# Optimization experiments

Measured on AMD Instinct MI355X. Metric: run time of the kernel, lower is better.

## Reference

```python
import jax, jax.numpy as jnp
import numpy as np

B, S, D, H = 2, 2048, 1024, 16
HD = D // H


def setup_inputs() -> dict:
    key = jax.random.key(0)
    ks = jax.random.split(key, 12)
    s = 0.02
    inp = {
        "query": jax.random.normal(ks[0], (B, S, D), dtype=jnp.float32),
        "Wq": jax.random.normal(ks[1], (D, D), dtype=jnp.float32) * s,
        "bq": jnp.zeros((D,), jnp.float32),
        "Wk": jax.random.normal(ks[2], (D, D), dtype=jnp.float32) * s,
        "bk": jnp.zeros((D,), jnp.float32),
        "Wv": jax.random.normal(ks[3], (D, D), dtype=jnp.float32) * s,
        "bv": jnp.zeros((D,), jnp.float32),
        "Wo": jax.random.normal(ks[4], (D, D), dtype=jnp.float32) * s,
        "bo": jnp.zeros((D,), jnp.float32),
        "Wm1": jax.random.normal(ks[5], (D // 4, D), dtype=jnp.float32) * s,
        "bm1": jnp.zeros((D // 4,), jnp.float32),
        "Wm2": jax.random.normal(ks[6], (D, D // 4), dtype=jnp.float32) * s,
        "bm2": jnp.zeros((D,), jnp.float32),
        "dopamine": jnp.ones((1,), jnp.float32),
        "serotonin": jnp.ones((1,), jnp.float32),
        "norepinephrine": jnp.ones((1,), jnp.float32),
        "acetylcholine": jnp.ones((1,), jnp.float32),
        "attention_scale": jnp.ones((1,), jnp.float32),
        "attention_bias": jnp.zeros((1,), jnp.float32),
    }
    return inp


def reference(query, Wq, bq, Wk, bk, Wv, bv, Wo, bo, Wm1, bm1, Wm2, bm2,
              dopamine, serotonin, norepinephrine, acetylcholine,
              attention_scale, attention_bias):
    b, s, d = query.shape
    scale = HD ** -0.5
    split = lambda t: t.reshape(b, s, H, HD).transpose(0, 2, 1, 3)  # [b,h,s,hd]
    q = split(query @ Wq.T + bq)
    k = split(query @ Wk.T + bk)
    v = split(query @ Wv.T + bv)
    scores = jnp.einsum('bhqd,bhkd->bhqk', q, k) * scale
    w = jax.nn.softmax(scores, axis=-1)  # dropout=0 (eval)
    attn = jnp.einsum('bhqk,bhkd->bhqd', w, v)
    # neuromodulation MLP on flattened query, then combined scalar gate
    mod = jax.nn.relu(query @ Wm1.T + bm1) @ Wm2.T + bm2  # [b,s,d]
    gate = (dopamine + serotonin + norepinephrine + acetylcholine) / 4.0  # [1]
    neuro = split(mod * gate)  # [b,h,s,hd]
    attn = (attn * attention_scale + attention_bias) * (1.0 + neuro)
    out = attn.transpose(0, 2, 1, 3).reshape(b, s, d) @ Wo.T + bo
    return out
```

## Files before the change

kernel.cpp:

```cpp
#include <hip/hip_runtime.h>
#include <hip/hip_bf16.h>
#include <stdint.h>
#include <math.h>


typedef __attribute__((ext_vector_type(8))) short short8;
typedef __attribute__((ext_vector_type(8))) unsigned short ushort8;
typedef __attribute__((ext_vector_type(4))) float floatx4;

#define MFMA16(a, b, c) __builtin_amdgcn_mfma_f32_16x16x32_bf16(a, b, c, 0, 0, 0)

__device__ __forceinline__ unsigned short f2bf(float f) {
    union { float f; uint32_t u; } v; v.f = f;
    uint32_t r = v.u + 0x7fffu + ((v.u >> 16) & 1u);
    return (unsigned short)(r >> 16);
}
__device__ __forceinline__ float bf2f(unsigned short s) {
    union { uint32_t u; float f; } v; v.u = ((uint32_t)s) << 16;
    return v.f;
}
__device__ __forceinline__ uint32_t pk2(float a, float b) {
    __hip_bfloat162 t = __float22bfloat162_rn(make_float2(a, b));
    uint32_t u; __builtin_memcpy(&u, &t, 4); return u;
}

typedef const __attribute__((address_space(1))) void gvoid_t;
typedef __attribute__((address_space(3))) void lvoid_t;
__device__ __forceinline__ void gld16(const void* g, void* l) {
    __builtin_amdgcn_global_load_lds((gvoid_t*)g, (lvoid_t*)l, 16, 0, 0);
}

template<bool OUTBF>
__device__ __forceinline__ void gemm_core128(const unsigned short* __restrict__ A,
                                             const unsigned short* __restrict__ W,
                                             const float* __restrict__ bias,
                                             void* __restrict__ C,
                                             int N, int K, int bm, int bn,
                                             bool relu, float osc,
                                             unsigned short* __restrict__ vt)
{
    __shared__ __align__(16) unsigned short As[2][128][32];
    __shared__ __align__(16) unsigned short Ws[2][128][32];

    const int tid  = threadIdx.x;
    const int w    = tid >> 6, lane = tid & 63;
    const int ln   = lane & 15, quad = lane >> 4;
    const int wm   = (w >> 1) * 64, wn = (w & 1) * 64;

    floatx4 acc[4][4] = {};

    auto stage = [&](int k0, int bb) {
        #pragma unroll
        for (int i = 0; i < 4; i++) {
            const int t = w * 4 + i;
            if (t < 8) {
                const int r0  = t * 16;
                const int row = r0 + (lane >> 2);
                const int c   = (lane & 3) ^ ((row >> 1) & 3);
                gld16(&A[(size_t)(bm + row) * K + k0 + c * 8], &As[bb][r0][0]);
            } else {
                const int r0  = (t - 8) * 16;
                const int row = r0 + (lane >> 2);
                const int c   = (lane & 3) ^ ((row >> 1) & 3);
                gld16(&W[(size_t)(bn + row) * K + k0 + c * 8], &Ws[bb][r0][0]);
            }
        }
    };

    stage(0, 0);

    const int KI = K >> 5;
    for (int ki = 0; ki < KI; ki++) {
        const int bb = ki & 1;
        __syncthreads();
        if (ki + 1 < KI) stage((ki + 1) << 5, bb ^ 1);

        short8 af[4], bf[4];
        #pragma unroll
        for (int mt = 0; mt < 4; mt++) {
            const int row = wm + mt * 16 + ln;
            af[mt] = *(const short8*)&As[bb][row][(quad ^ ((row >> 1) & 3)) * 8];
        }
        #pragma unroll
        for (int nt = 0; nt < 4; nt++) {
            const int row = wn + nt * 16 + ln;
            bf[nt] = *(const short8*)&Ws[bb][row][(quad ^ ((row >> 1) & 3)) * 8];
        }
        #pragma unroll
        for (int mt = 0; mt < 4; mt++)
            #pragma unroll
            for (int nt = 0; nt < 4; nt++)
                acc[mt][nt] = MFMA16(af[mt], bf[nt], acc[mt][nt]);
    }

    float bv[4];
    #pragma unroll
    for (int nt = 0; nt < 4; nt++) bv[nt] = bias[bn + wn + nt * 16 + ln];

    if (vt != nullptr) {
        #pragma unroll
        for (int mt = 0; mt < 4; mt++) {
            const int rowg = bm + wm + mt * 16 + quad * 4;
            const int b = rowg >> 11, s = rowg & 2047;
            #pragma unroll
            for (int nt = 0; nt < 4; nt++) {
                const int n = bn + wn + nt * 16 + ln;
                const int h = n >> 6, hd = n & 63;
                uint2 pk;
                pk.x = pk2(acc[mt][nt][0] + bv[nt], acc[mt][nt][1] + bv[nt]);
                pk.y = pk2(acc[mt][nt][2] + bv[nt], acc[mt][nt][3] + bv[nt]);
                *(uint2*)&vt[((size_t)(b * 16 + h) * 64 + hd) * 2048 + s] = pk;
            }
        }
        return;
    }

    #pragma unroll
    for (int mt = 0; mt < 4; mt++) {
        #pragma unroll
        for (int nt = 0; nt < 4; nt++) {
            #pragma unroll
            for (int r = 0; r < 4; r++) {
                float v = (acc[mt][nt][r] + bv[nt]) * osc;
                if (relu) v = fmaxf(v, 0.f);
                const size_t row = (size_t)bm + wm + mt * 16 + quad * 4 + r;
                const size_t col = (size_t)bn + wn + nt * 16 + ln;
                if (OUTBF) ((unsigned short*)C)[row * N + col] = f2bf(v);
                else       ((float*)C)[row * N + col] = v;
            }
        }
    }
}

template<bool OUTBF>
__device__ __forceinline__ void gemm_core64(const unsigned short* __restrict__ A,
                                            const unsigned short* __restrict__ W,
                                            const float* __restrict__ bias,
                                            void* __restrict__ C,
                                            int N, int K, int bm, int bn)
{
    __shared__ __align__(16) unsigned short As[2][128][64];
    __shared__ __align__(16) unsigned short Ws[2][64][64];

    const int tid  = threadIdx.x;
    const int w    = tid >> 6, lane = tid & 63;
    const int ln   = lane & 15, quad = lane >> 4;
    const int wm   = w * 32;

    floatx4 acc[2][4] = {};

    auto stage = [&](int k0, int bb) {
        #pragma unroll
        for (int i = 0; i < 6; i++) {
            const int t = w * 6 + i;
            if (t < 16) {
                const int row = t * 8 + (lane >> 3);
                const int c   = (lane & 7) ^ (row & 7);
                gld16(&A[(size_t)(bm + row) * K + k0 + c * 8], &As[bb][t * 8][0]);
            } else {
                const int tv  = t - 16;
                const int row = tv * 8 + (lane >> 3);
                const int c   = (lane & 7) ^ (row & 7);
                gld16(&W[(size_t)(bn + row) * K + k0 + c * 8], &Ws[bb][tv * 8][0]);
            }
        }
    };

    stage(0, 0);

    const int KI = K >> 6;
    for (int ki = 0; ki < KI; ki++) {
        const int bb = ki & 1;
        __syncthreads();
        if (ki + 1 < KI) stage((ki + 1) << 6, bb ^ 1);

        short8 af[2][2], bf[4][2];
        #pragma unroll
        for (int mt = 0; mt < 2; mt++) {
            const int row = wm + mt * 16 + ln;
            #pragma unroll
            for (int s = 0; s < 2; s++)
                af[mt][s] = *(const short8*)&As[bb][row][(((s * 4 + quad)) ^ (row & 7)) * 8];
        }
        #pragma unroll
        for (int nt = 0; nt < 4; nt++) {
            const int row = nt * 16 + ln;
            #pragma unroll
            for (int s = 0; s < 2; s++)
                bf[nt][s] = *(const short8*)&Ws[bb][row][(((s * 4 + quad)) ^ (row & 7)) * 8];
        }
        #pragma unroll
        for (int s = 0; s < 2; s++)
            #pragma unroll
            for (int mt = 0; mt < 2; mt++)
                #pragma unroll
                for (int nt = 0; nt < 4; nt++)
                    acc[mt][nt] = MFMA16(af[mt][s], bf[nt][s], acc[mt][nt]);
    }

    float bv[4];
    #pragma unroll
    for (int nt = 0; nt < 4; nt++) bv[nt] = bias[bn + nt * 16 + ln];

    #pragma unroll
    for (int mt = 0; mt < 2; mt++) {
        #pragma unroll
        for (int nt = 0; nt < 4; nt++) {
            #pragma unroll
            for (int r = 0; r < 4; r++) {
                const float v = acc[mt][nt][r] + bv[nt];
                const size_t row = (size_t)bm + wm + mt * 16 + quad * 4 + r;
                const size_t col = (size_t)bn + nt * 16 + ln;
                if (OUTBF) ((unsigned short*)C)[row * N + col] = f2bf(v);
                else       ((float*)C)[row * N + col] = v;
            }
        }
    }
}

#define QSCALE (0.125f * 1.44269504088896f)

__global__ __launch_bounds__(256) void qkv_mlp1_gemm(
    const unsigned short* __restrict__ A,
    const unsigned short* __restrict__ Wq, const unsigned short* __restrict__ Wk,
    const unsigned short* __restrict__ Wv, const unsigned short* __restrict__ Wm1,
    const float* __restrict__ bq, const float* __restrict__ bk,
    const float* __restrict__ bv, const float* __restrict__ bm1,
    unsigned short* __restrict__ Qo, unsigned short* __restrict__ Ko,
    unsigned short* __restrict__ Vt, unsigned short* __restrict__ Ho)
{
    const int flat = blockIdx.x + 26 * blockIdx.y;
    const int g = flat & 7, s = flat >> 3;
    const int bx = (g & 1) * 13 + (s % 13);
    const int bm = ((g >> 1) * 8 + (s / 13)) * 128;

    const unsigned short* W; const float* bias; unsigned short* C = nullptr;
    unsigned short* vt = nullptr;
    int N, bn; bool relu = false; float osc = 1.f;
    if (bx < 8)       { W = Wq;  bias = bq;  C = Qo; N = 1024; bn = bx * 128; osc = QSCALE; }
    else if (bx < 16) { W = Wk;  bias = bk;  C = Ko; N = 1024; bn = (bx - 8) * 128; }
    else if (bx < 24) { W = Wv;  bias = bv;  vt = Vt; N = 1024; bn = (bx - 16) * 128; }
    else              { W = Wm1; bias = bm1; C = Ho; N = 256;  bn = (bx - 24) * 128; relu = true; }
    gemm_core128<true>(A, W, bias, C, N, 1024, bm, bn, relu, osc, vt);
}

template<bool OUTBF>
__global__ __launch_bounds__(256) void gemm_bn64(const unsigned short* __restrict__ A,
                                                 const unsigned short* __restrict__ W,
                                                 const float* __restrict__ bias,
                                                 void* __restrict__ C, int N, int K)
{
    const int flat = blockIdx.x + 16 * blockIdx.y;
    const int g = flat & 7, s = flat >> 3;
    const int bx = (g & 1) * 8 + (s & 7);
    const int bm = ((g >> 1) * 8 + (s >> 3)) * 128;
    gemm_core64<OUTBF>(A, W, bias, C, N, K, bm, bx * 64);
}


__global__ __launch_bounds__(256) void attn_mfma(const unsigned short* __restrict__ Qg,
                                                 const unsigned short* __restrict__ Kg,
                                                 const unsigned short* __restrict__ Vtg,
                                                 const unsigned short* __restrict__ Modg,
                                                 unsigned short* __restrict__ Yg,
                                                 const float* __restrict__ dop,
                                                 const float* __restrict__ ser,
                                                 const float* __restrict__ nor,
                                                 const float* __restrict__ ach,
                                                 const float* __restrict__ asc,
                                                 const float* __restrict__ abi)
{
    __shared__ __align__(16) unsigned short Ks[2][128][64];
    __shared__ __align__(16) unsigned short Vs[2][64][128];
    __shared__ __align__(16) unsigned short Ps[4][2][16][64];

    const int tid = threadIdx.x;
    const int w   = tid >> 6, lane = tid & 63;
    const int ln  = lane & 15, quad = lane >> 4;
    const int h   = blockIdx.x, qt = blockIdx.y, b = blockIdx.z;

    const size_t kbase = (size_t)b * 2048 * 1024 + h * 64;
    const size_t vbase = (size_t)(b * 16 + h) * 64 * 2048;

    const size_t qrowbase = (size_t)b * 2048 + qt * 128 + w * 32;
    short8 qf[2][2];
    #pragma unroll
    for (int q2 = 0; q2 < 2; q2++) {
        const unsigned short* qp = Qg + (qrowbase + q2 * 16 + ln) * 1024 + h * 64;
        qf[q2][0] = *(const short8*)&qp[quad * 8];
        qf[q2][1] = *(const short8*)&qp[32 + quad * 8];
    }

    short8 ones8;
    #pragma unroll
    for (int j = 0; j < 8; j++) ones8[j] = (short)0x3F80;

    floatx4 o[2][4] = {};
    floatx4 ls[2] = {};

    auto stage = [&](int kc, int bb) {
        #pragma unroll
        for (int i = 0; i < 8; i++) {
            const int t = w * 8 + i;
            if (t < 16) {
                const int R = t * 8 + (lane >> 3);
                const int c = (lane & 7) ^ (R & 7);
                gld16(&Kg[kbase + (size_t)(kc * 128 + R) * 1024 + c * 8], &Ks[bb][t * 8][0]);
            } else {
                const int tv = t - 16;
                const int R  = tv * 4 + (lane >> 4);
                const int c  = (lane & 15) ^ (R & 15);
                gld16(&Vtg[vbase + (size_t)R * 2048 + kc * 128 + c * 8], &Vs[bb][tv * 4][0]);
            }
        }
    };

    stage(0, 0);

    for (int kc = 0; kc < 16; kc++) {
        const int bb = kc & 1;
        __syncthreads();
        if (kc + 1 < 16) stage(kc + 1, bb ^ 1);

        #pragma unroll
        for (int half = 0; half < 2; half++) {
            short8 kf[4][2];
            #pragma unroll
            for (int mt = 0; mt < 4; mt++) {
                const int row = half * 64 + mt * 16 + ln;
                kf[mt][0] = *(const short8*)&Ks[bb][row][((0 + quad) ^ (ln & 7)) * 8];
                kf[mt][1] = *(const short8*)&Ks[bb][row][((4 + quad) ^ (ln & 7)) * 8];
            }

            #pragma unroll
            for (int q2 = 0; q2 < 2; q2++) {
                floatx4 sc[4];
                #pragma unroll
                for (int mt = 0; mt < 4; mt++) {
                    floatx4 z = {};
                    z = MFMA16(kf[mt][0], qf[q2][0], z);
                    z = MFMA16(kf[mt][1], qf[q2][1], z);
                    sc[mt] = z;
                }
                #pragma unroll
                for (int mt = 0; mt < 4; mt++) {
                    const float p0 = __builtin_amdgcn_exp2f(sc[mt][0]);
                    const float p1 = __builtin_amdgcn_exp2f(sc[mt][1]);
                    const float p2 = __builtin_amdgcn_exp2f(sc[mt][2]);
                    const float p3 = __builtin_amdgcn_exp2f(sc[mt][3]);
                    uint2 pk; pk.x = pk2(p0, p1); pk.y = pk2(p2, p3);
                    const int c2 = (mt * 2 + (quad >> 1)) ^ (ln & 7);
                    *(uint2*)((char*)&Ps[w][q2][ln][0] + c2 * 16 + (quad & 1) * 8) = pk;
                }
            }

            short8 pf[2][2];
            #pragma unroll
            for (int q2 = 0; q2 < 2; q2++)
                #pragma unroll
                for (int ks = 0; ks < 2; ks++) {
                    const int c2 = (ks * 4 + quad) ^ (ln & 7);
                    pf[q2][ks] = *(const short8*)((char*)&Ps[w][q2][ln][0] + c2 * 16);
                }
            #pragma unroll
            for (int q2 = 0; q2 < 2; q2++)
                #pragma unroll
                for (int ks = 0; ks < 2; ks++)
                    ls[q2] = MFMA16(pf[q2][ks], ones8, ls[q2]);
            #pragma unroll
            for (int ntv = 0; ntv < 4; ntv++) {
                const int vrow = ntv * 16 + ln;
                #pragma unroll
                for (int ks = 0; ks < 2; ks++) {
                    const int c2 = (half * 8 + ks * 4 + quad) ^ (ln & 15);
                    const short8 vf = *(const short8*)&Vs[bb][vrow][c2 * 8];
                    o[0][ntv] = MFMA16(pf[0][ks], vf, o[0][ntv]);
                    o[1][ntv] = MFMA16(pf[1][ks], vf, o[1][ntv]);
                }
            }
        }
    }

    const float gate = 0.25f * (dop[0] + ser[0] + nor[0] + ach[0]);
    const float scb = asc[0], bib = abi[0];
    #pragma unroll
    for (int q2 = 0; q2 < 2; q2++) {
        #pragma unroll
        for (int r = 0; r < 4; r++) {
            const float inv = 1.f / ls[q2][r];
            const size_t row = qrowbase + q2 * 16 + quad * 4 + r;
            #pragma unroll
            for (int ntv = 0; ntv < 4; ntv++) {
                const size_t col = (size_t)h * 64 + ntv * 16 + ln;
                const float x  = o[q2][ntv][r] * inv;
                const float mo = bf2f(Modg[row * 1024 + col]);
                const float y  = (x * scb + bib) * (1.f + mo * gate);
                Yg[row * 1024 + col] = f2bf(y);
            }
        }
    }
}

__global__ __launch_bounds__(256) void fused_cast(
    const float* __restrict__ q,   const float* __restrict__ wq,
    const float* __restrict__ wk,  const float* __restrict__ wv,
    const float* __restrict__ wo,  const float* __restrict__ wm1,
    const float* __restrict__ wm2,
    unsigned short* __restrict__ dq,  unsigned short* __restrict__ dwq,
    unsigned short* __restrict__ dwk, unsigned short* __restrict__ dwv,
    unsigned short* __restrict__ dwo, unsigned short* __restrict__ dwm1,
    unsigned short* __restrict__ dwm2)
{
    const size_t u = (size_t)blockIdx.x * 256 + threadIdx.x;
    const float* src; unsigned short* dst; size_t off;
    if      (u <  524288) { src = q;   dst = dq;   off = u; }
    else if (u <  655360) { src = wq;  dst = dwq;  off = u - 524288; }
    else if (u <  786432) { src = wk;  dst = dwk;  off = u - 655360; }
    else if (u <  917504) { src = wv;  dst = dwv;  off = u - 786432; }
    else if (u < 1048576) { src = wo;  dst = dwo;  off = u - 917504; }
    else if (u < 1081344) { src = wm1; dst = dwm1; off = u - 1048576; }
    else                  { src = wm2; dst = dwm2; off = u - 1081344; }
    const float4* p = (const float4*)src + off * 2;
    const float4 a = p[0], c = p[1];
    uint4 o;
    o.x = pk2(a.x, a.y); o.y = pk2(a.z, a.w);
    o.z = pk2(c.x, c.y); o.w = pk2(c.z, c.w);
    *(uint4*)&dst[off * 8] = o;
}

extern "C" void kernel_launch(void* const* d_in, const int* in_sizes, int n_in,
                              void* d_out, int out_size, void* d_ws, size_t ws_size,
                              hipStream_t stream)
{
    const float* query = (const float*)d_in[0];
    const float* Wq  = (const float*)d_in[1];
    const float* bq  = (const float*)d_in[2];
    const float* Wk  = (const float*)d_in[3];
    const float* bk  = (const float*)d_in[4];
    const float* Wv  = (const float*)d_in[5];
    const float* bv  = (const float*)d_in[6];
    const float* Wo  = (const float*)d_in[7];
    const float* bo  = (const float*)d_in[8];
    const float* Wm1 = (const float*)d_in[9];
    const float* bm1 = (const float*)d_in[10];
    const float* Wm2 = (const float*)d_in[11];
    const float* bm2 = (const float*)d_in[12];
    const float* dop = (const float*)d_in[13];
    const float* ser = (const float*)d_in[14];
    const float* nor = (const float*)d_in[15];
    const float* ach = (const float*)d_in[16];
    const float* asc = (const float*)d_in[17];
    const float* abi = (const float*)d_in[18];

    char* ws = (char*)d_ws;
    const size_t MB = 1024 * 1024;
    unsigned short* Qry  = (unsigned short*)(ws);
    unsigned short* Wqb  = (unsigned short*)(ws + 8 * MB);
    unsigned short* Wkb  = (unsigned short*)(ws + 10 * MB);
    unsigned short* Wvb  = (unsigned short*)(ws + 12 * MB);
    unsigned short* Wob  = (unsigned short*)(ws + 14 * MB);
    unsigned short* Wm1b = (unsigned short*)(ws + 16 * MB);
    unsigned short* Wm2b = (unsigned short*)(ws + 16 * MB + 512 * 1024);
    unsigned short* Qb   = (unsigned short*)(ws + 17 * MB);
    unsigned short* Kb   = (unsigned short*)(ws + 25 * MB);
    unsigned short* Modb = (unsigned short*)(ws + 33 * MB);
    unsigned short* Vt   = (unsigned short*)(ws + 41 * MB);
    unsigned short* Yb   = (unsigned short*)(ws + 49 * MB);
    unsigned short* Hm   = (unsigned short*)(ws + 57 * MB);

    fused_cast<<<4352, 256, 0, stream>>>(query, Wq, Wk, Wv, Wo, Wm1, Wm2,
                                         Qry, Wqb, Wkb, Wvb, Wob, Wm1b, Wm2b);

    qkv_mlp1_gemm<<<dim3(26, 32), 256, 0, stream>>>(
        Qry, Wqb, Wkb, Wvb, Wm1b, bq, bk, bv, bm1, Qb, Kb, Vt, Hm);

    gemm_bn64<true><<<dim3(16, 32), 256, 0, stream>>>(Hm, Wm2b, bm2, (void*)Modb, 1024, 256);

    attn_mfma<<<dim3(16, 16, 2), 256, 0, stream>>>(Qb, Kb, Vt, Modb, Yb,
                                                   dop, ser, nor, ach, asc, abi);

    gemm_bn64<false><<<dim3(16, 32), 256, 0, stream>>>(Yb, Wob, bo, d_out, 1024, 1024);
}
```

Before: 227.5 us.

## Fuse second MLP GEMM into attention epilogue, drop separate Mod kernel

The Wm2 projection (Hm @ Wm2^T + bm2) is now computed inside the attention kernel's epilogue. Each block stages its head's 64 rows of Wm2 and its 128 query rows of Hm into the reused K/V shared buffers, then runs MFMAs directly into registers. This removes one kernel launch and the write and read of the bf16 Mod tensor, and keeps Mod in fp32 instead of rounding it to bf16. In exchange it adds a serialized GEMM tail to each attention block with no overlap, plus extra syncs and shared-memory reloads.

Result: faster. 220.2 us (-3.2%).

```diff
diff --git a/kernel.cpp b/kernel.cpp
--- a/kernel.cpp
+++ b/kernel.cpp
@@ -257,11 +257,12 @@
     gemm_core64<OUTBF>(A, W, bias, C, N, K, bm, bx * 64);
 }
 
-
 __global__ __launch_bounds__(256) void attn_mfma(const unsigned short* __restrict__ Qg,
                                                  const unsigned short* __restrict__ Kg,
                                                  const unsigned short* __restrict__ Vtg,
-                                                 const unsigned short* __restrict__ Modg,
+                                                 const unsigned short* __restrict__ Hmg,
+                                                 const unsigned short* __restrict__ Wm2g,
+                                                 const float* __restrict__ bm2,
                                                  unsigned short* __restrict__ Yg,
                                                  const float* __restrict__ dop,
                                                  const float* __restrict__ ser,
@@ -281,8 +282,9 @@
 
     const size_t kbase = (size_t)b * 2048 * 1024 + h * 64;
     const size_t vbase = (size_t)(b * 16 + h) * 64 * 2048;
-
-    const size_t qrowbase = (size_t)b * 2048 + qt * 128 + w * 32;
+    const size_t qtblk = (size_t)b * 2048 + qt * 128;
+
+    const size_t qrowbase = qtblk + w * 32;
     short8 qf[2][2];
     #pragma unroll
     for (int q2 = 0; q2 < 2; q2++) {
@@ -381,8 +383,73 @@
         }
     }
 
+    unsigned short* HmS = &Ks[0][0][0];
+    unsigned short* WmS = &Vs[0][0][0];
+
+    __syncthreads();
+
+    #pragma unroll
+    for (int i = 0; i < 8; i++) {
+        const int t  = w * 8 + i;
+        const int r0 = t * 2;
+        const int row = r0 + (lane >> 5);
+        const int sl  = lane & 31;
+        gld16(&Wm2g[(size_t)(h * 64 + row) * 256 + ((sl ^ (row & 7)) * 8)],
+              &WmS[r0 * 256]);
+    }
+    #pragma unroll
+    for (int i = 0; i < 8; i++) {
+        const int t  = w * 8 + i;
+        const int r0 = t * 4;
+        const int row = r0 + (lane >> 4);
+        const int sl  = lane & 15;
+        gld16(&Hmg[(qtblk + row) * 256 + ((sl ^ (row & 7)) * 8)],
+              &HmS[r0 * 128]);
+    }
+
+    floatx4 mo[2][4] = {};
+    #pragma unroll
+    for (int round = 0; round < 2; round++) {
+        __syncthreads();
+        if (round == 1) {
+        }
+        #pragma unroll
+        for (int ks = 0; ks < 4; ks++) {
+            short8 af[2];
+            #pragma unroll
+            for (int q2 = 0; q2 < 2; q2++) {
+                const int row = w * 32 + q2 * 16 + ln;
+                af[q2] = *(const short8*)&HmS[row * 128 + (((ks * 4 + quad) ^ (ln & 7)) * 8)];
+            }
+            #pragma unroll
+            for (int ntv = 0; ntv < 4; ntv++) {
+                const int row = ntv * 16 + ln;
+                const int ks8 = round * 4 + ks;
+                const short8 bf = *(const short8*)&WmS[row * 256 + (((ks8 * 4 + quad) ^ (ln & 7)) * 8)];
+                mo[0][ntv] = MFMA16(af[0], bf, mo[0][ntv]);
+                mo[1][ntv] = MFMA16(af[1], bf, mo[1][ntv]);
+            }
+        }
+        if (round == 0) {
+            __syncthreads();
+            #pragma unroll
+            for (int i = 0; i < 8; i++) {
+                const int t  = w * 8 + i;
+                const int r0 = t * 4;
+                const int row = r0 + (lane >> 4);
+                const int sl  = lane & 15;
+                gld16(&Hmg[(qtblk + row) * 256 + 128 + ((sl ^ (row & 7)) * 8)],
+                      &HmS[r0 * 128]);
+            }
+        }
+    }
+
     const float gate = 0.25f * (dop[0] + ser[0] + nor[0] + ach[0]);
     const float scb = asc[0], bib = abi[0];
+    float bm2v[4];
+    #pragma unroll
+    for (int ntv = 0; ntv < 4; ntv++) bm2v[ntv] = bm2[h * 64 + ntv * 16 + ln];
+
     #pragma unroll
     for (int q2 = 0; q2 < 2; q2++) {
         #pragma unroll
@@ -393,8 +460,8 @@
             for (int ntv = 0; ntv < 4; ntv++) {
                 const size_t col = (size_t)h * 64 + ntv * 16 + ln;
                 const float x  = o[q2][ntv][r] * inv;
-                const float mo = bf2f(Modg[row * 1024 + col]);
-                const float y  = (x * scb + bib) * (1.f + mo * gate);
+                const float m  = mo[q2][ntv][r] + bm2v[ntv];
+                const float y  = (x * scb + bib) * (1.f + m * gate);
                 Yg[row * 1024 + col] = f2bf(y);
             }
         }
@@ -463,7 +530,6 @@
     unsigned short* Wm2b = (unsigned short*)(ws + 16 * MB + 512 * 1024);
     unsigned short* Qb   = (unsigned short*)(ws + 17 * MB);
     unsigned short* Kb   = (unsigned short*)(ws + 25 * MB);
-    unsigned short* Modb = (unsigned short*)(ws + 33 * MB);
     unsigned short* Vt   = (unsigned short*)(ws + 41 * MB);
     unsigned short* Yb   = (unsigned short*)(ws + 49 * MB);
     unsigned short* Hm   = (unsigned short*)(ws + 57 * MB);
@@ -474,9 +540,7 @@
     qkv_mlp1_gemm<<<dim3(26, 32), 256, 0, stream>>>(
         Qry, Wqb, Wkb, Wvb, Wm1b, bq, bk, bv, bm1, Qb, Kb, Vt, Hm);
 
-    gemm_bn64<true><<<dim3(16, 32), 256, 0, stream>>>(Hm, Wm2b, bm2, (void*)Modb, 1024, 256);
-
-    attn_mfma<<<dim3(16, 16, 2), 256, 0, stream>>>(Qb, Kb, Vt, Modb, Yb,
+    attn_mfma<<<dim3(16, 16, 2), 256, 0, stream>>>(Qb, Kb, Vt, Hm, Wm2b, bm2, Yb,
                                                    dop, ser, nor, ach, asc, abi);
 
     gemm_bn64<false><<<dim3(16, 32), 256, 0, stream>>>(Yb, Wob, bo, d_out, 1024, 1024);
```
